# Kernel tuning notes

Measured on AMD Instinct MI355X. Metric: run time of the kernel, lower is better.

## Reference

```python
import jax, jax.numpy as jnp
import numpy as np

N_NODES = 10000
N_RAND_EDGES = 320000
IN_DIM = 256
HIDDEN = 64
HEADS = 8
OUT_DIM = 256
NEG_SLOPE = 0.2


def setup_inputs() -> dict:
    key = jax.random.key(0)
    ks = jax.random.split(key, 9)
    h = jax.random.normal(ks[0], (N_NODES, IN_DIM), dtype=jnp.float32)
    # random edges + self-loops so every dst has >=1 incoming edge
    src = jnp.concatenate([
        jax.random.randint(ks[1], (N_RAND_EDGES,), 0, N_NODES, dtype=jnp.int32),
        jnp.arange(N_NODES, dtype=jnp.int32)])
    dst = jnp.concatenate([
        jax.random.randint(ks[2], (N_RAND_EDGES,), 0, N_NODES, dtype=jnp.int32),
        jnp.arange(N_NODES, dtype=jnp.int32)])
    def glorot(k, shape):
        fan = shape[0] + shape[-1]
        s = jnp.sqrt(2.0 / fan).astype(jnp.float32)
        return jax.random.normal(k, shape, dtype=jnp.float32) * s
    W1 = glorot(ks[3], (IN_DIM, HEADS * HIDDEN))
    attn_l1 = glorot(ks[4], (HEADS, HIDDEN))
    attn_r1 = glorot(ks[5], (HEADS, HIDDEN))
    W2 = glorot(ks[6], (HEADS * HIDDEN, OUT_DIM))
    attn_l2 = glorot(ks[7], (1, OUT_DIM))
    attn_r2 = glorot(ks[8], (1, OUT_DIM))
    return {"h": h, "W1": W1, "attn_l1": attn_l1, "attn_r1": attn_r1,
            "W2": W2, "attn_l2": attn_l2, "attn_r2": attn_r2,
            "src": src, "dst": dst}


def gat_conv(x, W, attn_l, attn_r, src, dst, n_nodes):
    # x: [N, F_in]; W: [F_in, H*D]; attn_l/attn_r: [H, D]
    H, D = attn_l.shape
    feat = (x @ W).reshape(n_nodes, H, D)          # [N, H, D]
    el = jnp.einsum('nhd,hd->nh', feat, attn_l)    # [N, H]
    er = jnp.einsum('nhd,hd->nh', feat, attn_r)
    e = jax.nn.leaky_relu(el[src] + er[dst], NEG_SLOPE)  # [E, H]
    # edge softmax over incoming edges of each destination node
    m = jax.ops.segment_max(e, dst, num_segments=n_nodes)      # [N, H]
    ex = jnp.exp(e - m[dst])                                   # [E, H]
    denom = jax.ops.segment_sum(ex, dst, num_segments=n_nodes) # [N, H]
    alpha = ex / denom[dst]                                    # [E, H]
    out = jax.ops.segment_sum(alpha[:, :, None] * feat[src], dst,
                              num_segments=n_nodes)            # [N, H, D]
    return out.reshape(n_nodes, H * D)


def reference(h, W1, attn_l1, attn_r1, W2, attn_l2, attn_r2, src, dst):
    n = h.shape[0]
    x = gat_conv(h, W1, attn_l1, attn_r1, src, dst, n)   # [N, H*hidden]
    x = jax.nn.elu(x)
    out = gat_conv(x, W2, attn_l2, attn_r2, src, dst, n) # [N, out_dim]
    return out
```

## Files before the change

### kernel.cpp

```cpp
#include <hip/hip_runtime.h>
#include <hip/hip_bf16.h>

#define N_NODES 10000
#define IN_DIM 256
#define HID 512
#define HEADS 8
#define OUT_DIM 256
#define NEG 0.2f
#define CAP 128

typedef __hip_bfloat16 bf16;
typedef __attribute__((ext_vector_type(8))) short short8;
typedef __attribute__((ext_vector_type(4))) float f32x4;

__device__ __forceinline__ float ldm(const void* p, long i, int mode){
  if(mode) return ((const float*)p)[i];
  return __bfloat162float(((const bf16*)p)[i]);
}
__device__ __forceinline__ unsigned short f2bf(float f){
  bf16 b = __float2bfloat16(f);
  return *(unsigned short*)&b;
}
__device__ __forceinline__ float bflo(unsigned int u){ return __uint_as_float(u<<16); }
__device__ __forceinline__ float bfhi(unsigned int u){ return __uint_as_float(u&0xffff0000u); }

__global__ void detect_zero_k(const unsigned short* w1raw, int* mode, int* cnt,
                              float* el1, float* er1, float* el2, float* er2){
  int t = threadIdx.x;
  if(blockIdx.x==0){
    __shared__ int sbad;
    if(t==0) sbad=0;
    __syncthreads();
    int bad=0;
    for(int i=t;i<512;i+=256){
      unsigned int u = ((unsigned int)w1raw[i])<<16;
      float f = __uint_as_float(u);
      if(!(f==f) || fabsf(f) > 100.0f) bad++;
    }
    #pragma unroll
    for(int o=32;o>0;o>>=1) bad += __shfl_down(bad,o);
    if((t&63)==0) atomicAdd(&sbad, bad);
    __syncthreads();
    if(t==0) *mode = (sbad>10) ? 1 : 0;
  } else {
    int i = (blockIdx.x-1)*256 + t;
    if(i<N_NODES*HEADS){ el1[i]=0.f; er1[i]=0.f; }
    if(i<N_NODES){ cnt[i]=0; el2[i]=0.f; er2[i]=0.f; }
  }
}

__global__ void scatter_k(const int* src, const int* dst, int* cnt, int* bucket, int E){
  int e = blockIdx.x*256 + threadIdx.x;
  if(e<E){
    int d = dst[e];
    int pos = atomicAdd(&cnt[d], 1);
    if(pos < CAP) bucket[(long)d*CAP + pos] = src[e];
  }
}

__global__ void wprep_k(const void* W1, const void* W2, unsigned short* wt1,
                        unsigned short* wt2, const int* modep){
  int md = *modep;
  long i = (long)blockIdx.x*256 + threadIdx.x;
  const long n1 = (long)IN_DIM*HID;
  if(i < n1){
    int k = (int)(i/HID), n = (int)(i%HID);
    unsigned short v = md ? f2bf(((const float*)W1)[i]) : ((const unsigned short*)W1)[i];
    wt1[(long)n*IN_DIM + k] = v;
  } else {
    long j = i - n1;
    int k = (int)(j/OUT_DIM), n = (int)(j%OUT_DIM);
    unsigned short v = md ? f2bf(((const float*)W2)[j]) : ((const unsigned short*)W2)[j];
    wt2[(long)n*HID + k] = v;
  }
}

__global__ __launch_bounds__(256) void gemm_k(const void* A, const unsigned short* Bt,
                                              unsigned short* C, int M, int N, int K,
                                              int asel, const int* modep,
                                              const void* al, const void* ar,
                                              float* el, float* er, int dmode){
  int md = *modep;
  int am = asel ? md : 0;
  __shared__ short As[64*40];
  __shared__ short Bs[64*40];
  __shared__ float led[64], ler[64];
  int t = threadIdx.x;
  int lane = t & 63, wave = t >> 6;
  int l15 = lane & 15, quad = lane >> 4;
  int wm = (wave>>1)*32, wn = (wave&1)*32;
  int mbase = blockIdx.y*64, nbase = blockIdx.x*64;

  f32x4 acc[2][2];
  #pragma unroll
  for(int i=0;i<2;i++)
    #pragma unroll
    for(int j=0;j<2;j++) acc[i][j] = (f32x4){0.f,0.f,0.f,0.f};

  int row = t>>2, kk = (t&3)*8;
  long arow = (long)(mbase+row)*K, brow = (long)(nbase+row)*K;
  bool av = (mbase+row) < M;
  const unsigned short* Ab = (const unsigned short*)A;
  const float* Af = (const float*)A;

  for(int k0=0;k0<K;k0+=32){
    short8 a = (short8){0,0,0,0,0,0,0,0};
    if(am){
      if(av){
        float4 x = *(const float4*)(Af + arow + k0 + kk);
        float4 y = *(const float4*)(Af + arow + k0 + kk + 4);
        a[0]=f2bf(x.x); a[1]=f2bf(x.y); a[2]=f2bf(x.z); a[3]=f2bf(x.w);
        a[4]=f2bf(y.x); a[5]=f2bf(y.y); a[6]=f2bf(y.z); a[7]=f2bf(y.w);
      }
    } else {
      if(av) a = *(const short8*)(Ab + arow + k0 + kk);
    }
    short8 b = *(const short8*)(Bt + brow + k0 + kk);
    __syncthreads();
    *(short8*)(As + row*40 + kk) = a;
    *(short8*)(Bs + row*40 + kk) = b;
    __syncthreads();
    short8 af[2], bfr[2];
    #pragma unroll
    for(int mi=0;mi<2;mi++) af[mi]  = *(short8*)(As + (wm + mi*16 + l15)*40 + quad*8);
    #pragma unroll
    for(int ni=0;ni<2;ni++) bfr[ni] = *(short8*)(Bs + (wn + ni*16 + l15)*40 + quad*8);
    #pragma unroll
    for(int mi=0;mi<2;mi++)
      #pragma unroll
      for(int ni=0;ni<2;ni++)
        acc[mi][ni] = __builtin_amdgcn_mfma_f32_16x16x32_bf16(af[mi], bfr[ni], acc[mi][ni], 0,0,0);
  }

  #pragma unroll
  for(int mi=0;mi<2;mi++){
    #pragma unroll
    for(int ni=0;ni<2;ni++){
      int grow0 = mbase + wm + mi*16 + quad*4;
      int gcol  = nbase + wn + ni*16 + l15;
      #pragma unroll
      for(int r=0;r<4;r++){
        int grow = grow0 + r;
        if(grow < M) C[(long)grow*N + gcol] = f2bf(acc[mi][ni][r]);
      }
    }
  }

  float avv[2], rvv[2];
  #pragma unroll
  for(int ni=0;ni<2;ni++){
    int gc = nbase + wn + ni*16 + l15;
    avv[ni] = ldm(al, gc, md);
    rvv[ni] = ldm(ar, gc, md);
  }
  __syncthreads();
  if(t<64){ led[t]=0.f; ler[t]=0.f; }
  __syncthreads();
  #pragma unroll
  for(int mi=0;mi<2;mi++){
    #pragma unroll
    for(int r=0;r<4;r++){
      float pl = acc[mi][0][r]*avv[0] + acc[mi][1][r]*avv[1];
      float pr = acc[mi][0][r]*rvv[0] + acc[mi][1][r]*rvv[1];
      #pragma unroll
      for(int o=1;o<16;o<<=1){ pl += __shfl_xor(pl,o); pr += __shfl_xor(pr,o); }
      if(l15==0){
        int lr = wm + mi*16 + quad*4 + r;
        atomicAdd(&led[lr], pl);
        atomicAdd(&ler[lr], pr);
      }
    }
  }
  __syncthreads();
  if(t<64){
    int grow = mbase + t;
    if(grow < M){
      int estride = (dmode==1) ? HEADS : 1;
      int hidx    = (dmode==1) ? (nbase>>6) : 0;
      atomicAdd(&el[(long)grow*estride + hidx], led[t]);
      atomicAdd(&er[(long)grow*estride + hidx], ler[t]);
    }
  }
}

__global__ __launch_bounds__(128) void agg1_k(const unsigned short* fb, const float* el,
                       const float* er, const int* cnt, const int* bucket, unsigned short* x){
  int n = blockIdx.x, t = threadIdx.x;
  long off = (long)n*CAP;
  int deg = cnt[n]; if(deg>CAP) deg=CAP;
  __shared__ float wsum[8], ers[8];
  __shared__ int sidx[CAP];
  __shared__ float wlds[CAP*8];
  if(t<8){ wsum[t]=0.f; ers[t]=er[n*HEADS+t]; }
  for(int i=t;i<deg;i+=128) sidx[i]=bucket[off+i];
  __syncthreads();
  {
    int tot = deg*HEADS;
    float pw = 0.f;
    int myh = t&7;
    float erh = ers[myh];
    for(int p=t; p<tot; p+=128){
      int i = p>>3;
      int s = sidx[i];
      float e = el[s*HEADS+myh] + erh;
      e = e>0.f ? e : NEG*e;
      float w = __expf(e);
      wlds[p]=w;
      pw += w;
    }
    #pragma unroll
    for(int o=32;o>=8;o>>=1) pw += __shfl_xor(pw,o);
    if((t&63)<8) atomicAdd(&wsum[t&63], pw);
  }
  __syncthreads();
  if(t<8) wsum[t] = wsum[t]>0.f ? 1.f/wsum[t] : 0.f;
  __syncthreads();
  int c0 = 4*t;
  int h = t>>4;
  float inv = wsum[h];
  float a0=0.f,a1=0.f,a2=0.f,a3=0.f;
  #pragma unroll 4
  for(int i=0;i<deg;i++){
    int s = sidx[i];
    float w = wlds[i*8+h];
    uint2 u = *(const uint2*)(fb + (long)s*HID + c0);
    a0 += w*bflo(u.x); a1 += w*bfhi(u.x);
    a2 += w*bflo(u.y); a3 += w*bfhi(u.y);
  }
  a0*=inv; a1*=inv; a2*=inv; a3*=inv;
  a0 = a0>0.f ? a0 : __expf(a0)-1.f;
  a1 = a1>0.f ? a1 : __expf(a1)-1.f;
  a2 = a2>0.f ? a2 : __expf(a2)-1.f;
  a3 = a3>0.f ? a3 : __expf(a3)-1.f;
  uint2 o2;
  o2.x = (unsigned int)f2bf(a0) | ((unsigned int)f2bf(a1)<<16);
  o2.y = (unsigned int)f2bf(a2) | ((unsigned int)f2bf(a3)<<16);
  *(uint2*)(x + (long)n*HID + c0) = o2;
}

__global__ __launch_bounds__(64) void agg2_k(const unsigned short* fb, const float* el,
                       const float* er, const int* cnt, const int* bucket, void* out,
                       const int* modep){
  int md = *modep;
  int n = blockIdx.x, t = threadIdx.x;
  long off = (long)n*CAP;
  int deg = cnt[n]; if(deg>CAP) deg=CAP;
  __shared__ int sidx[CAP];
  __shared__ float wlds[CAP];
  for(int i=t;i<deg;i+=64) sidx[i]=bucket[off+i];
  __syncthreads();
  float ern = er[n];
  float pw = 0.f;
  for(int i=t; i<deg; i+=64){
    int s = sidx[i];
    float e = el[s]+ern; e = e>0.f ? e : NEG*e;
    float w = __expf(e);
    wlds[i]=w;
    pw += w;
  }
  #pragma unroll
  for(int o=32;o>0;o>>=1) pw += __shfl_xor(pw,o);
  float inv = pw>0.f ? 1.f/pw : 0.f;
  __syncthreads();
  int c0 = 4*t;
  float a0=0.f,a1=0.f,a2=0.f,a3=0.f;
  #pragma unroll 4
  for(int i=0;i<deg;i++){
    int s = sidx[i];
    float w = wlds[i];
    uint2 u = *(const uint2*)(fb + (long)s*OUT_DIM + c0);
    a0 += w*bflo(u.x); a1 += w*bfhi(u.x);
    a2 += w*bflo(u.y); a3 += w*bfhi(u.y);
  }
  a0*=inv; a1*=inv; a2*=inv; a3*=inv;
  long oi = (long)n*OUT_DIM + c0;
  if(md){
    float4 fo; fo.x=a0; fo.y=a1; fo.z=a2; fo.w=a3;
    *(float4*)((float*)out + oi) = fo;
  } else {
    uint2 o2;
    o2.x = (unsigned int)f2bf(a0) | ((unsigned int)f2bf(a1)<<16);
    o2.y = (unsigned int)f2bf(a2) | ((unsigned int)f2bf(a3)<<16);
    *(uint2*)((unsigned short*)out + oi) = o2;
  }
}

extern "C" void kernel_launch(void* const* d_in, const int* in_sizes, int n_in,
                              void* d_out, int out_size, void* d_ws, size_t ws_size,
                              hipStream_t stream){
  (void)n_in; (void)out_size; (void)ws_size;
  const void* h_in = d_in[0];
  const void* W1   = d_in[1];
  const void* al1  = d_in[2];
  const void* ar1  = d_in[3];
  const void* W2   = d_in[4];
  const void* al2  = d_in[5];
  const void* ar2  = d_in[6];
  const int* src = (const int*)d_in[7];
  const int* dst = (const int*)d_in[8];
  int E = in_sizes[7];

  char* ws = (char*)d_ws;
  size_t o = 0;
  auto alloc = [&](size_t b){ size_t c=o; o += (b+255)&~(size_t)255; return c; };
  unsigned short* f1b  = (unsigned short*)(ws + alloc((size_t)N_NODES*HID*2));
  unsigned short* f2b  = (unsigned short*)(ws + alloc((size_t)N_NODES*OUT_DIM*2));
  unsigned short* xbuf = (unsigned short*)(ws + alloc((size_t)N_NODES*HID*2));
  unsigned short* wt1  = (unsigned short*)(ws + alloc((size_t)IN_DIM*HID*2));
  unsigned short* wt2  = (unsigned short*)(ws + alloc((size_t)HID*OUT_DIM*2));
  float* el1   = (float*)(ws + alloc((size_t)N_NODES*HEADS*4));
  float* er1   = (float*)(ws + alloc((size_t)N_NODES*HEADS*4));
  float* el2   = (float*)(ws + alloc((size_t)N_NODES*4));
  float* er2   = (float*)(ws + alloc((size_t)N_NODES*4));
  int* cnt     = (int*)(ws + alloc((size_t)N_NODES*4));
  int* bucket  = (int*)(ws + alloc((size_t)N_NODES*CAP*4));
  int* modep   = (int*)(ws + alloc(256));

  detect_zero_k<<<1+(N_NODES*HEADS+255)/256,256,0,stream>>>(
      (const unsigned short*)W1, modep, cnt, el1, er1, el2, er2);
  scatter_k<<<(E+255)/256,256,0,stream>>>(src, dst, cnt, bucket, E);
  wprep_k<<<(int)(((long)IN_DIM*HID+(long)HID*OUT_DIM)/256),256,0,stream>>>(W1, W2, wt1, wt2, modep);

  gemm_k<<<dim3(HID/64,(N_NODES+63)/64),256,0,stream>>>(
      h_in, wt1, f1b, N_NODES, HID, IN_DIM, 1, modep, al1, ar1, el1, er1, 1);
  agg1_k<<<N_NODES,128,0,stream>>>(f1b, el1, er1, cnt, bucket, xbuf);

  gemm_k<<<dim3(OUT_DIM/64,(N_NODES+63)/64),256,0,stream>>>(
      xbuf, wt2, f2b, N_NODES, OUT_DIM, HID, 0, modep, al2, ar2, el2, er2, 2);
  agg2_k<<<N_NODES,64,0,stream>>>(f2b, el2, er2, cnt, bucket, d_out, modep);
}
```

Measured before the change: 194.0 us.

## Split aggregation blocks across head pairs and column halves; merge prep kernels

The scatter and weight-transpose kernels are merged into one launch to save a kernel launch. Both aggregation kernels now split each destination node across several blocks. agg1 uses four blocks per node, each handling two heads with 64 threads, and agg2 uses two blocks per column half. This raises parallelism and shrinks per-block work, but the bucket loads and attention-weight computation are repeated in every block, and each thread now does narrower 4-byte gathers instead of 8-byte ones.

Measured after the change: 189.6 us. 1.02x faster.

```diff
diff --git a/kernel.cpp b/kernel.cpp
--- a/kernel.cpp
+++ b/kernel.cpp
@@ -8,6 +8,7 @@
 #define OUT_DIM 256
 #define NEG 0.2f
 #define CAP 128
+#define WPREP_BLOCKS (((IN_DIM*HID)+(HID*OUT_DIM))/256)
 
 typedef __hip_bfloat16 bf16;
 typedef __attribute__((ext_vector_type(8))) short short8;
@@ -49,29 +50,31 @@
   }
 }
 
-__global__ void scatter_k(const int* src, const int* dst, int* cnt, int* bucket, int E){
-  int e = blockIdx.x*256 + threadIdx.x;
-  if(e<E){
-    int d = dst[e];
-    int pos = atomicAdd(&cnt[d], 1);
-    if(pos < CAP) bucket[(long)d*CAP + pos] = src[e];
-  }
-}
-
-__global__ void wprep_k(const void* W1, const void* W2, unsigned short* wt1,
-                        unsigned short* wt2, const int* modep){
-  int md = *modep;
-  long i = (long)blockIdx.x*256 + threadIdx.x;
-  const long n1 = (long)IN_DIM*HID;
-  if(i < n1){
-    int k = (int)(i/HID), n = (int)(i%HID);
-    unsigned short v = md ? f2bf(((const float*)W1)[i]) : ((const unsigned short*)W1)[i];
-    wt1[(long)n*IN_DIM + k] = v;
+__global__ void prep2_k(const void* W1, const void* W2, unsigned short* wt1,
+                        unsigned short* wt2, const int* modep,
+                        const int* src, const int* dst, int* cnt, int* bucket, int E){
+  int b = blockIdx.x, t = threadIdx.x;
+  if(b < WPREP_BLOCKS){
+    int md = *modep;
+    long i = (long)b*256 + t;
+    const long n1 = (long)IN_DIM*HID;
+    if(i < n1){
+      int k = (int)(i/HID), n = (int)(i%HID);
+      unsigned short v = md ? f2bf(((const float*)W1)[i]) : ((const unsigned short*)W1)[i];
+      wt1[(long)n*IN_DIM + k] = v;
+    } else {
+      long j = i - n1;
+      int k = (int)(j/OUT_DIM), n = (int)(j%OUT_DIM);
+      unsigned short v = md ? f2bf(((const float*)W2)[j]) : ((const unsigned short*)W2)[j];
+      wt2[(long)n*HID + k] = v;
+    }
   } else {
-    long j = i - n1;
-    int k = (int)(j/OUT_DIM), n = (int)(j%OUT_DIM);
-    unsigned short v = md ? f2bf(((const float*)W2)[j]) : ((const unsigned short*)W2)[j];
-    wt2[(long)n*HID + k] = v;
+    int e = (b-WPREP_BLOCKS)*256 + t;
+    if(e<E){
+      int d = dst[e];
+      int pos = atomicAdd(&cnt[d], 1);
+      if(pos < CAP) bucket[(long)d*CAP + pos] = src[e];
+    }
   }
 }
 
@@ -183,105 +186,96 @@
   }
 }
 
-__global__ __launch_bounds__(128) void agg1_k(const unsigned short* fb, const float* el,
+__global__ __launch_bounds__(64) void agg1_k(const unsigned short* fb, const float* el,
                        const float* er, const int* cnt, const int* bucket, unsigned short* x){
-  int n = blockIdx.x, t = threadIdx.x;
+  int b = blockIdx.x;
+  int hp = b / N_NODES;
+  int n  = b - hp*N_NODES;
+  int t = threadIdx.x;
   long off = (long)n*CAP;
   int deg = cnt[n]; if(deg>CAP) deg=CAP;
-  __shared__ float wsum[8], ers[8];
   __shared__ int sidx[CAP];
-  __shared__ float wlds[CAP*8];
-  if(t<8){ wsum[t]=0.f; ers[t]=er[n*HEADS+t]; }
-  for(int i=t;i<deg;i+=128) sidx[i]=bucket[off+i];
-  __syncthreads();
-  {
-    int tot = deg*HEADS;
-    float pw = 0.f;
-    int myh = t&7;
-    float erh = ers[myh];
-    for(int p=t; p<tot; p+=128){
-      int i = p>>3;
-      int s = sidx[i];
-      float e = el[s*HEADS+myh] + erh;
-      e = e>0.f ? e : NEG*e;
-      float w = __expf(e);
-      wlds[p]=w;
-      pw += w;
-    }
-    #pragma unroll
-    for(int o=32;o>=8;o>>=1) pw += __shfl_xor(pw,o);
-    if((t&63)<8) atomicAdd(&wsum[t&63], pw);
-  }
-  __syncthreads();
-  if(t<8) wsum[t] = wsum[t]>0.f ? 1.f/wsum[t] : 0.f;
-  __syncthreads();
-  int c0 = 4*t;
-  int h = t>>4;
-  float inv = wsum[h];
-  float a0=0.f,a1=0.f,a2=0.f,a3=0.f;
+  __shared__ float w0[CAP], w1[CAP];
+  for(int i=t;i<deg;i+=64) sidx[i]=bucket[off+i];
+  __syncthreads();
+  int h0 = 2*hp;
+  float er0 = er[n*HEADS+h0], er1 = er[n*HEADS+h0+1];
+  float pw0=0.f, pw1=0.f;
+  for(int i=t;i<deg;i+=64){
+    int s = sidx[i];
+    float2 ev = *(const float2*)(el + (long)s*HEADS + h0);
+    float e0 = ev.x + er0; e0 = e0>0.f?e0:NEG*e0;
+    float e1 = ev.y + er1; e1 = e1>0.f?e1:NEG*e1;
+    float wa = __expf(e0), wb = __expf(e1);
+    w0[i]=wa; w1[i]=wb;
+    pw0+=wa; pw1+=wb;
+  }
+  #pragma unroll
+  for(int o=32;o>0;o>>=1){ pw0 += __shfl_xor(pw0,o); pw1 += __shfl_xor(pw1,o); }
+  float inv0 = pw0>0.f?1.f/pw0:0.f, inv1 = pw1>0.f?1.f/pw1:0.f;
+  __syncthreads();
+  int c0 = hp*128 + 2*t;
+  const float* wsel = (t<32)? w0 : w1;
+  float inv = (t<32)? inv0 : inv1;
+  float a0=0.f, a1=0.f;
   #pragma unroll 4
   for(int i=0;i<deg;i++){
     int s = sidx[i];
-    float w = wlds[i*8+h];
-    uint2 u = *(const uint2*)(fb + (long)s*HID + c0);
-    a0 += w*bflo(u.x); a1 += w*bfhi(u.x);
-    a2 += w*bflo(u.y); a3 += w*bfhi(u.y);
-  }
-  a0*=inv; a1*=inv; a2*=inv; a3*=inv;
+    float w = wsel[i];
+    unsigned int u = *(const unsigned int*)(fb + (long)s*HID + c0);
+    a0 += w*bflo(u); a1 += w*bfhi(u);
+  }
+  a0*=inv; a1*=inv;
   a0 = a0>0.f ? a0 : __expf(a0)-1.f;
   a1 = a1>0.f ? a1 : __expf(a1)-1.f;
-  a2 = a2>0.f ? a2 : __expf(a2)-1.f;
-  a3 = a3>0.f ? a3 : __expf(a3)-1.f;
-  uint2 o2;
-  o2.x = (unsigned int)f2bf(a0) | ((unsigned int)f2bf(a1)<<16);
-  o2.y = (unsigned int)f2bf(a2) | ((unsigned int)f2bf(a3)<<16);
-  *(uint2*)(x + (long)n*HID + c0) = o2;
+  *(unsigned int*)(x + (long)n*HID + c0) =
+      (unsigned int)f2bf(a0) | ((unsigned int)f2bf(a1)<<16);
 }
 
 __global__ __launch_bounds__(64) void agg2_k(const unsigned short* fb, const float* el,
                        const float* er, const int* cnt, const int* bucket, void* out,
                        const int* modep){
   int md = *modep;
-  int n = blockIdx.x, t = threadIdx.x;
+  int b = blockIdx.x;
+  int ch = b / N_NODES;
+  int n  = b - ch*N_NODES;
+  int t = threadIdx.x;
   long off = (long)n*CAP;
   int deg = cnt[n]; if(deg>CAP) deg=CAP;
   __shared__ int sidx[CAP];
-  __shared__ float wlds[CAP];
+  __shared__ float wl[CAP];
   for(int i=t;i<deg;i+=64) sidx[i]=bucket[off+i];
   __syncthreads();
   float ern = er[n];
   float pw = 0.f;
-  for(int i=t; i<deg; i+=64){
+  for(int i=t;i<deg;i+=64){
     int s = sidx[i];
     float e = el[s]+ern; e = e>0.f ? e : NEG*e;
     float w = __expf(e);
-    wlds[i]=w;
+    wl[i]=w;
     pw += w;
   }
   #pragma unroll
   for(int o=32;o>0;o>>=1) pw += __shfl_xor(pw,o);
   float inv = pw>0.f ? 1.f/pw : 0.f;
   __syncthreads();
-  int c0 = 4*t;
-  float a0=0.f,a1=0.f,a2=0.f,a3=0.f;
+  int c0 = ch*128 + 2*t;
+  float a0=0.f, a1=0.f;
   #pragma unroll 4
   for(int i=0;i<deg;i++){
     int s = sidx[i];
-    float w = wlds[i];
-    uint2 u = *(const uint2*)(fb + (long)s*OUT_DIM + c0);
-    a0 += w*bflo(u.x); a1 += w*bfhi(u.x);
-    a2 += w*bflo(u.y); a3 += w*bfhi(u.y);
-  }
-  a0*=inv; a1*=inv; a2*=inv; a3*=inv;
+    float w = wl[i];
+    unsigned int u = *(const unsigned int*)(fb + (long)s*OUT_DIM + c0);
+    a0 += w*bflo(u); a1 += w*bfhi(u);
+  }
+  a0*=inv; a1*=inv;
   long oi = (long)n*OUT_DIM + c0;
   if(md){
-    float4 fo; fo.x=a0; fo.y=a1; fo.z=a2; fo.w=a3;
-    *(float4*)((float*)out + oi) = fo;
+    float2 fo; fo.x=a0; fo.y=a1;
+    *(float2*)((float*)out + oi) = fo;
   } else {
-    uint2 o2;
-    o2.x = (unsigned int)f2bf(a0) | ((unsigned int)f2bf(a1)<<16);
-    o2.y = (unsigned int)f2bf(a2) | ((unsigned int)f2bf(a3)<<16);
-    *(uint2*)((unsigned short*)out + oi) = o2;
+    *(unsigned int*)((unsigned short*)out + oi) =
+        (unsigned int)f2bf(a0) | ((unsigned int)f2bf(a1)<<16);
   }
 }
 
@@ -318,14 +312,14 @@
 
   detect_zero_k<<<1+(N_NODES*HEADS+255)/256,256,0,stream>>>(
       (const unsigned short*)W1, modep, cnt, el1, er1, el2, er2);
-  scatter_k<<<(E+255)/256,256,0,stream>>>(src, dst, cnt, bucket, E);
-  wprep_k<<<(int)(((long)IN_DIM*HID+(long)HID*OUT_DIM)/256),256,0,stream>>>(W1, W2, wt1, wt2, modep);
+  prep2_k<<<WPREP_BLOCKS+(E+255)/256,256,0,stream>>>(
+      W1, W2, wt1, wt2, modep, src, dst, cnt, bucket, E);
 
   gemm_k<<<dim3(HID/64,(N_NODES+63)/64),256,0,stream>>>(
       h_in, wt1, f1b, N_NODES, HID, IN_DIM, 1, modep, al1, ar1, el1, er1, 1);
-  agg1_k<<<N_NODES,128,0,stream>>>(f1b, el1, er1, cnt, bucket, xbuf);
+  agg1_k<<<4*N_NODES,64,0,stream>>>(f1b, el1, er1, cnt, bucket, xbuf);
 
   gemm_k<<<dim3(OUT_DIM/64,(N_NODES+63)/64),256,0,stream>>>(
       xbuf, wt2, f2b, N_NODES, OUT_DIM, HID, 0, modep, al2, ar2, el2, er2, 2);
-  agg2_k<<<N_NODES,64,0,stream>>>(f2b, el2, er2, cnt, bucket, d_out, modep);
-}
+  agg2_k<<<2*N_NODES,64,0,stream>>>(f2b, el2, er2, cnt, bucket, d_out, modep);
+}
```

## Split layer-1 aggregation into head-halves, merge prep kernels, drop el1 atomics

Applied to the files above, without the earlier changes.

The layer-1 aggregation now launches two 64-thread blocks per node, each covering four heads (256 columns), with a per-head weight array in shared memory and wave-level reductions instead of shared atomics. The scatter and weight-transpose kernels are merged into one launch. The first GEMM writes el1/er1 directly, since each column block maps to exactly one head, so the zeroing of el1/er1 in the init kernel is removed. This aims to raise parallelism, shorten the aggregation's synchronisation, and cut launches and atomics, at the cost of loading each node's bucket indices twice.

After: 184.5 us, median of 2. 4.9% less time.

```diff
diff --git a/kernel.cpp b/kernel.cpp
--- a/kernel.cpp
+++ b/kernel.cpp
@@ -8,6 +8,7 @@
 #define OUT_DIM 256
 #define NEG 0.2f
 #define CAP 128
+#define WPREP_BLOCKS (((IN_DIM*HID)+(HID*OUT_DIM))/256)
 
 typedef __hip_bfloat16 bf16;
 typedef __attribute__((ext_vector_type(8))) short short8;
@@ -25,7 +26,7 @@
 __device__ __forceinline__ float bfhi(unsigned int u){ return __uint_as_float(u&0xffff0000u); }
 
 __global__ void detect_zero_k(const unsigned short* w1raw, int* mode, int* cnt,
-                              float* el1, float* er1, float* el2, float* er2){
+                              float* el2, float* er2){
   int t = threadIdx.x;
   if(blockIdx.x==0){
     __shared__ int sbad;
@@ -44,34 +45,35 @@
     if(t==0) *mode = (sbad>10) ? 1 : 0;
   } else {
     int i = (blockIdx.x-1)*256 + t;
-    if(i<N_NODES*HEADS){ el1[i]=0.f; er1[i]=0.f; }
     if(i<N_NODES){ cnt[i]=0; el2[i]=0.f; er2[i]=0.f; }
   }
 }
 
-__global__ void scatter_k(const int* src, const int* dst, int* cnt, int* bucket, int E){
-  int e = blockIdx.x*256 + threadIdx.x;
-  if(e<E){
-    int d = dst[e];
-    int pos = atomicAdd(&cnt[d], 1);
-    if(pos < CAP) bucket[(long)d*CAP + pos] = src[e];
-  }
-}
-
-__global__ void wprep_k(const void* W1, const void* W2, unsigned short* wt1,
-                        unsigned short* wt2, const int* modep){
-  int md = *modep;
-  long i = (long)blockIdx.x*256 + threadIdx.x;
-  const long n1 = (long)IN_DIM*HID;
-  if(i < n1){
-    int k = (int)(i/HID), n = (int)(i%HID);
-    unsigned short v = md ? f2bf(((const float*)W1)[i]) : ((const unsigned short*)W1)[i];
-    wt1[(long)n*IN_DIM + k] = v;
+__global__ void prep2_k(const void* W1, const void* W2, unsigned short* wt1,
+                        unsigned short* wt2, const int* modep,
+                        const int* src, const int* dst, int* cnt, int* bucket, int E){
+  int b = blockIdx.x, t = threadIdx.x;
+  if(b < WPREP_BLOCKS){
+    int md = *modep;
+    long i = (long)b*256 + t;
+    const long n1 = (long)IN_DIM*HID;
+    if(i < n1){
+      int k = (int)(i/HID), n = (int)(i%HID);
+      unsigned short v = md ? f2bf(((const float*)W1)[i]) : ((const unsigned short*)W1)[i];
+      wt1[(long)n*IN_DIM + k] = v;
+    } else {
+      long j = i - n1;
+      int k = (int)(j/OUT_DIM), n = (int)(j%OUT_DIM);
+      unsigned short v = md ? f2bf(((const float*)W2)[j]) : ((const unsigned short*)W2)[j];
+      wt2[(long)n*HID + k] = v;
+    }
   } else {
-    long j = i - n1;
-    int k = (int)(j/OUT_DIM), n = (int)(j%OUT_DIM);
-    unsigned short v = md ? f2bf(((const float*)W2)[j]) : ((const unsigned short*)W2)[j];
-    wt2[(long)n*HID + k] = v;
+    int e = (b-WPREP_BLOCKS)*256 + t;
+    if(e<E){
+      int d = dst[e];
+      int pos = atomicAdd(&cnt[d], 1);
+      if(pos < CAP) bucket[(long)d*CAP + pos] = src[e];
+    }
   }
 }
 
@@ -175,54 +177,61 @@
   if(t<64){
     int grow = mbase + t;
     if(grow < M){
-      int estride = (dmode==1) ? HEADS : 1;
-      int hidx    = (dmode==1) ? (nbase>>6) : 0;
-      atomicAdd(&el[(long)grow*estride + hidx], led[t]);
-      atomicAdd(&er[(long)grow*estride + hidx], ler[t]);
-    }
-  }
-}
-
-__global__ __launch_bounds__(128) void agg1_k(const unsigned short* fb, const float* el,
+      if(dmode==1){
+        el[(long)grow*HEADS + blockIdx.x] = led[t];
+        er[(long)grow*HEADS + blockIdx.x] = ler[t];
+      } else {
+        atomicAdd(&el[grow], led[t]);
+        atomicAdd(&er[grow], ler[t]);
+      }
+    }
+  }
+}
+
+__global__ __launch_bounds__(64) void agg1_k(const unsigned short* fb, const float* el,
                        const float* er, const int* cnt, const int* bucket, unsigned short* x){
-  int n = blockIdx.x, t = threadIdx.x;
+  int b = blockIdx.x;
+  int ch = b / N_NODES;
+  int n  = b - ch*N_NODES;
+  int t = threadIdx.x;
   long off = (long)n*CAP;
   int deg = cnt[n]; if(deg>CAP) deg=CAP;
-  __shared__ float wsum[8], ers[8];
   __shared__ int sidx[CAP];
-  __shared__ float wlds[CAP*8];
-  if(t<8){ wsum[t]=0.f; ers[t]=er[n*HEADS+t]; }
-  for(int i=t;i<deg;i+=128) sidx[i]=bucket[off+i];
-  __syncthreads();
-  {
-    int tot = deg*HEADS;
-    float pw = 0.f;
-    int myh = t&7;
-    float erh = ers[myh];
-    for(int p=t; p<tot; p+=128){
-      int i = p>>3;
-      int s = sidx[i];
-      float e = el[s*HEADS+myh] + erh;
-      e = e>0.f ? e : NEG*e;
-      float w = __expf(e);
-      wlds[p]=w;
-      pw += w;
-    }
-    #pragma unroll
-    for(int o=32;o>=8;o>>=1) pw += __shfl_xor(pw,o);
-    if((t&63)<8) atomicAdd(&wsum[t&63], pw);
-  }
-  __syncthreads();
-  if(t<8) wsum[t] = wsum[t]>0.f ? 1.f/wsum[t] : 0.f;
-  __syncthreads();
-  int c0 = 4*t;
-  int h = t>>4;
-  float inv = wsum[h];
+  __shared__ float wl[4][CAP];
+  for(int i=t;i<deg;i+=64) sidx[i]=bucket[off+i];
+  __syncthreads();
+  int h0 = ch*4;
+  float4 erv = *(const float4*)(er + (long)n*HEADS + h0);
+  float pw0=0.f, pw1=0.f, pw2=0.f, pw3=0.f;
+  for(int i=t;i<deg;i+=64){
+    int s = sidx[i];
+    float4 ev = *(const float4*)(el + (long)s*HEADS + h0);
+    float e0 = ev.x + erv.x; e0 = e0>0.f?e0:NEG*e0;
+    float e1 = ev.y + erv.y; e1 = e1>0.f?e1:NEG*e1;
+    float e2 = ev.z + erv.z; e2 = e2>0.f?e2:NEG*e2;
+    float e3 = ev.w + erv.w; e3 = e3>0.f?e3:NEG*e3;
+    float wa = __expf(e0), wb = __expf(e1), wc = __expf(e2), wd = __expf(e3);
+    wl[0][i]=wa; wl[1][i]=wb; wl[2][i]=wc; wl[3][i]=wd;
+    pw0+=wa; pw1+=wb; pw2+=wc; pw3+=wd;
+  }
+  #pragma unroll
+  for(int o=32;o>0;o>>=1){
+    pw0 += __shfl_xor(pw0,o); pw1 += __shfl_xor(pw1,o);
+    pw2 += __shfl_xor(pw2,o); pw3 += __shfl_xor(pw3,o);
+  }
+  float invs[4];
+  invs[0] = pw0>0.f?1.f/pw0:0.f; invs[1] = pw1>0.f?1.f/pw1:0.f;
+  invs[2] = pw2>0.f?1.f/pw2:0.f; invs[3] = pw3>0.f?1.f/pw3:0.f;
+  __syncthreads();
+  int hl = t>>4;
+  int c0 = ch*256 + 4*t;
+  const float* wsel = wl[hl];
+  float inv = invs[hl];
   float a0=0.f,a1=0.f,a2=0.f,a3=0.f;
   #pragma unroll 4
   for(int i=0;i<deg;i++){
     int s = sidx[i];
-    float w = wlds[i*8+h];
+    float w = wsel[i];
     uint2 u = *(const uint2*)(fb + (long)s*HID + c0);
     a0 += w*bflo(u.x); a1 += w*bfhi(u.x);
     a2 += w*bflo(u.y); a3 += w*bfhi(u.y);
@@ -246,16 +255,16 @@
   long off = (long)n*CAP;
   int deg = cnt[n]; if(deg>CAP) deg=CAP;
   __shared__ int sidx[CAP];
-  __shared__ float wlds[CAP];
+  __shared__ float wl[CAP];
   for(int i=t;i<deg;i+=64) sidx[i]=bucket[off+i];
   __syncthreads();
   float ern = er[n];
   float pw = 0.f;
-  for(int i=t; i<deg; i+=64){
+  for(int i=t;i<deg;i+=64){
     int s = sidx[i];
     float e = el[s]+ern; e = e>0.f ? e : NEG*e;
     float w = __expf(e);
-    wlds[i]=w;
+    wl[i]=w;
     pw += w;
   }
   #pragma unroll
@@ -267,7 +276,7 @@
   #pragma unroll 4
   for(int i=0;i<deg;i++){
     int s = sidx[i];
-    float w = wlds[i];
+    float w = wl[i];
     uint2 u = *(const uint2*)(fb + (long)s*OUT_DIM + c0);
     a0 += w*bflo(u.x); a1 += w*bfhi(u.x);
     a2 += w*bflo(u.y); a3 += w*bfhi(u.y);
@@ -316,14 +325,14 @@
   int* bucket  = (int*)(ws + alloc((size_t)N_NODES*CAP*4));
   int* modep   = (int*)(ws + alloc(256));
 
-  detect_zero_k<<<1+(N_NODES*HEADS+255)/256,256,0,stream>>>(
-      (const unsigned short*)W1, modep, cnt, el1, er1, el2, er2);
-  scatter_k<<<(E+255)/256,256,0,stream>>>(src, dst, cnt, bucket, E);
-  wprep_k<<<(int)(((long)IN_DIM*HID+(long)HID*OUT_DIM)/256),256,0,stream>>>(W1, W2, wt1, wt2, modep);
+  detect_zero_k<<<1+(N_NODES+255)/256,256,0,stream>>>(
+      (const unsigned short*)W1, modep, cnt, el2, er2);
+  prep2_k<<<WPREP_BLOCKS+(E+255)/256,256,0,stream>>>(
+      W1, W2, wt1, wt2, modep, src, dst, cnt, bucket, E);
 
   gemm_k<<<dim3(HID/64,(N_NODES+63)/64),256,0,stream>>>(
       h_in, wt1, f1b, N_NODES, HID, IN_DIM, 1, modep, al1, ar1, el1, er1, 1);
-  agg1_k<<<N_NODES,128,0,stream>>>(f1b, el1, er1, cnt, bucket, xbuf);
+  agg1_k<<<2*N_NODES,64,0,stream>>>(f1b, el1, er1, cnt, bucket, xbuf);
 
   gemm_k<<<dim3(OUT_DIM/64,(N_NODES+63)/64),256,0,stream>>>(
       xbuf, wt2, f2b, N_NODES, OUT_DIM, HID, 0, modep, al2, ar2, el2, er2, 2);
```
